# Optimization experiments

Hardware: AMD Instinct MI355X
Metric: run time of the kernel (lower is better)

Reference implementation:

```python
import jax, jax.numpy as jnp
import numpy as np

B, H, W, C = 4, 512, 512, 64


def setup_inputs() -> dict:
    key = jax.random.key(0)
    k1, k2 = jax.random.split(key)
    image = jax.random.normal(k1, (B, H, W, C), dtype=jnp.float32)
    flow = jax.random.normal(k2, (B, H, W, 2), dtype=jnp.float32)
    return {"image": image, "flow": flow}


def _dense_image_warp(image, flow):
    # tfa.image.dense_image_warp: output[b,y,x,c] = image[b, y - flow[b,y,x,0], x - flow[b,y,x,1], c]
    # with bilinear interpolation; floors are clamped to [0, size-2], alphas to [0,1]
    b, h, w, c = image.shape
    grid_y = jnp.arange(h, dtype=flow.dtype)[None, :, None]   # [1,H,1]
    grid_x = jnp.arange(w, dtype=flow.dtype)[None, None, :]   # [1,1,W]
    qy = grid_y - flow[..., 0]                                # [B,H,W]
    qx = grid_x - flow[..., 1]                                # [B,H,W]

    fy = jnp.clip(jnp.floor(qy), 0.0, h - 2)
    fx = jnp.clip(jnp.floor(qx), 0.0, w - 2)
    ay = jnp.clip(qy - fy, 0.0, 1.0)[..., None]               # [B,H,W,1]
    ax = jnp.clip(qx - fx, 0.0, 1.0)[..., None]

    y0 = fy.astype(jnp.int32)
    x0 = fx.astype(jnp.int32)
    y1 = y0 + 1
    x1 = x0 + 1

    bidx = jnp.arange(b, dtype=jnp.int32)[:, None, None]      # [B,1,1]
    top_left = image[bidx, y0, x0]                            # [B,H,W,C]
    top_right = image[bidx, y0, x1]
    bottom_left = image[bidx, y1, x0]
    bottom_right = image[bidx, y1, x1]

    top = top_left + ax * (top_right - top_left)
    bottom = bottom_left + ax * (bottom_right - bottom_left)
    return top + ay * (bottom - top)


def reference(image, flow):
    return _dense_image_warp(image, flow)
```

## Files before the change

### kernel.cpp

```cpp
#include <hip/hip_runtime.h>


#define BB 4
#define HH 512
#define WW 512
#define CC 64
#define CV (CC / 4)
#define CT 8

typedef float f32x4 __attribute__((ext_vector_type(4)));

__global__ __launch_bounds__(256) void backwarp_kernel(
    const float* __restrict__ image,
    const float* __restrict__ flow,
    float* __restrict__ out)
{
    long long idx = (long long)blockIdx.x * 256 + threadIdx.x;
    int c8 = (int)(idx & (CT - 1));
    long long p = idx >> 3;
    int x = (int)(p & (WW - 1));
    long long t = p >> 9;
    int y = (int)(t & (HH - 1));
    int b = (int)(t >> 9);

    float2 fl = ((const float2*)flow)[p];
    float qy = (float)y - fl.x;
    float qx = (float)x - fl.y;

    float fy = fminf(fmaxf(floorf(qy), 0.0f), (float)(HH - 2));
    float fx = fminf(fmaxf(floorf(qx), 0.0f), (float)(WW - 2));
    float ay = fminf(fmaxf(qy - fy, 0.0f), 1.0f);
    float ax = fminf(fmaxf(qx - fx, 0.0f), 1.0f);
    int y0 = (int)fy;
    int x0 = (int)fx;

    const f32x4* img4 = (const f32x4*)image;
    long long i00 = (((long long)b * HH + y0) * WW + x0) * CV + c8;
    long long i01 = i00 + CV;
    long long i10 = i00 + (long long)WW * CV;
    long long i11 = i10 + CV;

    f32x4 tlA = img4[i00];     f32x4 tlB = img4[i00 + 8];
    f32x4 trA = img4[i01];     f32x4 trB = img4[i01 + 8];
    f32x4 blA = img4[i10];     f32x4 blB = img4[i10 + 8];
    f32x4 brA = img4[i11];     f32x4 brB = img4[i11 + 8];

    f32x4 topA = tlA + ax * (trA - tlA);
    f32x4 botA = blA + ax * (brA - blA);
    f32x4 rA   = topA + ay * (botA - topA);
    f32x4 topB = tlB + ax * (trB - tlB);
    f32x4 botB = blB + ax * (brB - blB);
    f32x4 rB   = topB + ay * (botB - topB);

    long long o = p * CV + c8;
    f32x4* out4 = (f32x4*)out;
    __builtin_nontemporal_store(rA, &out4[o]);
    __builtin_nontemporal_store(rB, &out4[o + 8]);
}

extern "C" void kernel_launch(void* const* d_in, const int* in_sizes, int n_in,
                              void* d_out, int out_size, void* d_ws, size_t ws_size,
                              hipStream_t stream) {
    const float* image = (const float*)d_in[0];
    const float* flow  = (const float*)d_in[1];
    float* out = (float*)d_out;

    const long long total = (long long)BB * HH * WW * CT;
    const int block = 256;
    const long long grid = total / block;

    backwarp_kernel<<<(unsigned)grid, block, 0, stream>>>(image, flow, out);
}
```

Measured before the change: 107.6 us.

## Process two pixel groups per thread with XCD-aware block remapping

Each block now handles 64 pixels instead of 32. Every thread warps two pixels, and both flow loads are issued up front with nontemporal hints. Block IDs are remapped so that round-robin dispatch across the chip's eight dies assigns contiguous pixel ranges to each die, which is meant to improve L2 locality for neighbouring gather reads. The cost is half as many blocks and more registers per thread, which could reduce latency hiding.

```diff
diff --git a/kernel.cpp b/kernel.cpp
--- a/kernel.cpp
+++ b/kernel.cpp
@@ -4,29 +4,23 @@
 #define BB 4
 #define HH 512
 #define WW 512
-#define CC 64
-#define CV (CC / 4)
-#define CT 8
+#define CV 16
+#define NBLK 16384
 
 typedef float f32x4 __attribute__((ext_vector_type(4)));
+typedef float f32x2 __attribute__((ext_vector_type(2)));
 
-__global__ __launch_bounds__(256) void backwarp_kernel(
-    const float* __restrict__ image,
-    const float* __restrict__ flow,
-    float* __restrict__ out)
+__device__ __forceinline__ void warp_body(
+    const f32x4* __restrict__ img4, f32x4* __restrict__ out4,
+    long long p, int c8, f32x2 fl)
 {
-    long long idx = (long long)blockIdx.x * 256 + threadIdx.x;
-    int c8 = (int)(idx & (CT - 1));
-    long long p = idx >> 3;
     int x = (int)(p & (WW - 1));
     long long t = p >> 9;
     int y = (int)(t & (HH - 1));
     int b = (int)(t >> 9);
 
-    float2 fl = ((const float2*)flow)[p];
     float qy = (float)y - fl.x;
     float qx = (float)x - fl.y;
-
     float fy = fminf(fmaxf(floorf(qy), 0.0f), (float)(HH - 2));
     float fx = fminf(fmaxf(floorf(qx), 0.0f), (float)(WW - 2));
     float ay = fminf(fmaxf(qy - fy, 0.0f), 1.0f);
@@ -34,16 +28,15 @@
     int y0 = (int)fy;
     int x0 = (int)fx;
 
-    const f32x4* img4 = (const f32x4*)image;
     long long i00 = (((long long)b * HH + y0) * WW + x0) * CV + c8;
     long long i01 = i00 + CV;
     long long i10 = i00 + (long long)WW * CV;
     long long i11 = i10 + CV;
 
-    f32x4 tlA = img4[i00];     f32x4 tlB = img4[i00 + 8];
-    f32x4 trA = img4[i01];     f32x4 trB = img4[i01 + 8];
-    f32x4 blA = img4[i10];     f32x4 blB = img4[i10 + 8];
-    f32x4 brA = img4[i11];     f32x4 brB = img4[i11 + 8];
+    f32x4 tlA = img4[i00];  f32x4 tlB = img4[i00 + 8];
+    f32x4 trA = img4[i01];  f32x4 trB = img4[i01 + 8];
+    f32x4 blA = img4[i10];  f32x4 blB = img4[i10 + 8];
+    f32x4 brA = img4[i11];  f32x4 brB = img4[i11 + 8];
 
     f32x4 topA = tlA + ax * (trA - tlA);
     f32x4 botA = blA + ax * (brA - blA);
@@ -53,9 +46,33 @@
     f32x4 rB   = topB + ay * (botB - topB);
 
     long long o = p * CV + c8;
-    f32x4* out4 = (f32x4*)out;
     __builtin_nontemporal_store(rA, &out4[o]);
     __builtin_nontemporal_store(rB, &out4[o + 8]);
+}
+
+__global__ __launch_bounds__(256) void backwarp_kernel(
+    const float* __restrict__ image,
+    const float* __restrict__ flow,
+    float* __restrict__ out)
+{
+    int bid = (int)blockIdx.x;
+    int orig = (bid & 7) * (NBLK / 8) + (bid >> 3);
+
+    long long pix_base = (long long)orig * 64;
+    int c8 = (int)(threadIdx.x & 7);
+    int pl = (int)(threadIdx.x >> 3);
+    long long p0 = pix_base + pl;
+    long long p1 = pix_base + 32 + pl;
+
+    const f32x2* flow2 = (const f32x2*)flow;
+    f32x2 fl0 = __builtin_nontemporal_load(&flow2[p0]);
+    f32x2 fl1 = __builtin_nontemporal_load(&flow2[p1]);
+
+    const f32x4* img4 = (const f32x4*)image;
+    f32x4* out4 = (f32x4*)out;
+
+    warp_body(img4, out4, p0, c8, fl0);
+    warp_body(img4, out4, p1, c8, fl1);
 }
 
 extern "C" void kernel_launch(void* const* d_in, const int* in_sizes, int n_in,
@@ -65,9 +82,5 @@
     const float* flow  = (const float*)d_in[1];
     float* out = (float*)d_out;
 
-    const long long total = (long long)BB * HH * WW * CT;
-    const int block = 256;
-    const long long grid = total / block;
-
-    backwarp_kernel<<<(unsigned)grid, block, 0, stream>>>(image, flow, out);
+    backwarp_kernel<<<NBLK, 256, 0, stream>>>(image, flow, out);
 }
```

After: 101.7 us. 5.4% less time.
